# Optimization experiments

Measured on AMD Instinct MI355X. Metric: run time of the kernel, lower is better.

## Reference

```python
import jax, jax.numpy as jnp
from jax import lax
import numpy as np

KERNEL = 3      # patch kernel
RATE = 2        # dilation / downscale rate
SCALE = 10.0    # softmax_scale
EPS = 1e-4


def extract_patches(x, k, s):
    """TF tf.image.extract_patches with SAME padding.
    x: [B,H,W,C] -> [B, oh, ow, k, k, C] with (ky,kx,c) ordering like TF depth."""
    B, H, W, C = x.shape
    oh, ow = -(-H // s), -(-W // s)
    ph = max((oh - 1) * s + k - H, 0)
    pw = max((ow - 1) * s + k - W, 0)
    xp = jnp.pad(x, ((0, 0), (ph // 2, ph - ph // 2), (pw // 2, pw - pw // 2), (0, 0)))
    rows = []
    for ky in range(k):
        cols = [xp[:, ky: ky + (oh - 1) * s + 1: s, kx: kx + (ow - 1) * s + 1: s, :]
                for kx in range(k)]
        rows.append(jnp.stack(cols, axis=3))        # [B,oh,ow,kx,C]
    return jnp.stack(rows, axis=3)                  # [B,oh,ow,ky,kx,C]


def resize_half(x):
    B, H, W, C = x.shape
    return jax.image.resize(x, (B, H // 2, W // 2, C), 'bilinear', antialias=False)


def fuse_diag(a):
    """conv2d of [N,N] image with eye(3) kernel (SAME): out[i,j]=a[i-1,j-1]+a[i,j]+a[i+1,j+1]."""
    p = jnp.pad(a, 1)
    return p[:-2, :-2] + p[1:-1, 1:-1] + p[2:, 2:]


def setup_inputs() -> dict:
    key = jax.random.key(0)
    x = jax.random.normal(key, (4, 96, 96, 128), jnp.float32)
    # binary mask with a central square hole (1 = missing region)
    mask = jnp.zeros((4, 96, 96, 1), jnp.float32).at[:, 24:72, 24:72, :].set(1.0)
    return {"x": x, "mask": mask}


def reference(x, mask):
    B, H, W, C = x.shape
    k, rate = KERNEL, RATE

    # raw patches from full-res x, stride rate -> deconv weights
    raw_p = extract_patches(x, k, rate)                     # [B,h,w,k,k,C]
    h, w = raw_p.shape[1], raw_p.shape[2]
    L = h * w
    raw_w = raw_p.reshape(B, L, k, k, C).transpose(0, 2, 3, 4, 1)   # [B,k,k,C,L]

    # downscaled foreground/background (f == b in this module) and mask
    f = resize_half(x)                                      # [B,h,w,C]
    m = resize_half(mask)                                   # [B,h,w,1]

    wp = extract_patches(f, k, 1).reshape(B, L, k, k, C).transpose(0, 2, 3, 4, 1)  # [B,k,k,C,L]
    mp = extract_patches(m, k, 1).reshape(B, L, -1)         # [B,L,k*k*1]
    mm = (jnp.mean(mp, axis=-1) == 0.0).astype(x.dtype)     # [B,L] valid-patch mask

    fp = extract_patches(f, k, 1)                           # [B,h,w,k,k,C] query patches

    def per_sample(fp_i, wi, raw_wi, mm_i):
        # normalized cross-correlation: conv2d(f_i, wi_normed, SAME)
        norm = jnp.maximum(jnp.sqrt(jnp.sum(wi * wi, axis=(0, 1, 2))), EPS)   # [L]
        wn = wi / norm
        yi = jnp.einsum('hwabc,abcl->hwl', fp_i, wn)        # [h,w,L]

        # diagonal fuse (eye(3) conv) on both patch-grid orderings
        a = fuse_diag(yi.reshape(L, L))
        a = a.reshape(h, w, h, w).transpose(1, 0, 3, 2).reshape(L, L)
        a = fuse_diag(a)
        a = a.reshape(w, h, w, h).transpose(1, 0, 3, 2)     # [h,w,h,w]
        yi = a.reshape(h, w, L)

        # masked softmax over source patches
        yi = yi * mm_i
        yi = jax.nn.softmax(yi * SCALE, axis=-1) * mm_i

        # conv2d_transpose(yi, raw_wi, [1,H,W,C], strides=rate) == vjp of strided conv
        def fwd(z):  # z: [H,W,C] -> [h,w,L]
            return lax.conv_general_dilated(z[None], raw_wi, (rate, rate), 'SAME',
                                            dimension_numbers=('NHWC', 'HWIO', 'NHWC'))[0]
        _, vjp = jax.vjp(fwd, jnp.zeros((H, W, C), x.dtype))
        return vjp(yi)[0] / (rate * rate)                   # [H,W,C]

    return jax.vmap(per_sample)(fp, wp, raw_w, mm)          # [B,H,W,C]
```

## Files before the change

### kernel.cpp

```cpp
#include <hip/hip_runtime.h>
#include <hip/hip_fp16.h>
#include <stdint.h>
#include <string.h>


namespace {

constexpr int B_ = 4;
constexpr int H_ = 96;
constexpr int W_ = 96;
constexpr int C_ = 128;
constexpr int h_ = 48;
constexpr int L_ = 2304;
constexpr int N9_ = 1152;
constexpr int K3_ = 384;
constexpr float SCALE_ = 10.0f;
constexpr float EPS_ = 1e-4f;

constexpr int OUT_F16 = 1;
constexpr int OUT_BF16 = 2;

typedef unsigned short u16;
typedef __attribute__((ext_vector_type(8))) short bfrag8;
typedef __attribute__((ext_vector_type(8))) unsigned short ushort8;
typedef __attribute__((ext_vector_type(4))) unsigned short ushort4v;
typedef __attribute__((ext_vector_type(4))) float f32x4;
typedef __attribute__((ext_vector_type(2))) float f32x2;

__device__ __forceinline__ u16 f2bf(float f) {
  uint32_t x;
  __builtin_memcpy(&x, &f, 4);
  uint32_t lsb = (x >> 16) & 1u;
  x += 0x7fffu + lsb;
  return (u16)(x >> 16);
}
__device__ __forceinline__ float bf2f(u16 u) {
  uint32_t v = ((uint32_t)u) << 16;
  float f;
  __builtin_memcpy(&f, &v, 4);
  return f;
}
__device__ __forceinline__ u16 f2h(float f) {
  __half h = __float2half(f);
  u16 u;
  __builtin_memcpy(&u, &h, 2);
  return u;
}
__device__ __forceinline__ float h2f(u16 u) {
  __half h;
  __builtin_memcpy(&h, &u, 2);
  return __half2float(h);
}

__device__ __forceinline__ void gload16(const u16* g, void* l) {
  __builtin_amdgcn_global_load_lds(
      (const __attribute__((address_space(1))) void*)g,
      (__attribute__((address_space(3))) void*)l, 16, 0, 0);
}

__device__ __forceinline__ int xcd_swz8(int orig, int nwg) {
  int q = nwg >> 3, r = nwg & 7;
  int xcd = orig & 7, pos = orig >> 3;
  return (xcd < r ? xcd * (q + 1) : r * (q + 1) + (xcd - r) * q) + pos;
}

__device__ __forceinline__ uint32_t swzb(uint32_t byte) {
  return byte ^ (((byte >> 7) & 7u) << 4);
}

__global__ __launch_bounds__(128) void k_down(const float* __restrict__ x,
                                              u16* __restrict__ F3a,
                                              u16* __restrict__ F3b,
                                              float* __restrict__ S) {
  int blk = blockIdx.x;
  int b = blk / L_, l = blk % L_;
  int p = l / h_, q = l % h_;
  int c = threadIdx.x;
  const float* xb = x + (((size_t)b * H_ + 2 * p) * W_ + 2 * q) * C_ + c;
  float v = 0.25f * (xb[0] + xb[C_] + xb[(size_t)W_ * C_] + xb[(size_t)W_ * C_ + C_]);
  u16 hi = f2bf(v);
  u16 lo = f2bf(v - bf2f(hi));
  size_t base = ((size_t)b * L_ + l) * K3_;
  F3a[base + c] = hi; F3a[base + 128 + c] = hi; F3a[base + 256 + c] = lo;
  F3b[base + c] = hi; F3b[base + 128 + c] = lo; F3b[base + 256 + c] = hi;
  float ss = v * v;
#pragma unroll
  for (int o = 32; o >= 1; o >>= 1) ss += __shfl_xor(ss, o, 64);
  __shared__ float w2[2];
  if ((c & 63) == 0) w2[c >> 6] = ss;
  __syncthreads();
  if (c == 0) S[(size_t)b * L_ + l] = w2[0] + w2[1];
}

__global__ __launch_bounds__(256) void k_mask(const float* __restrict__ mask,
                                              float* __restrict__ md) {
  int i = blockIdx.x * 256 + threadIdx.x;
  int b = i / L_, l = i % L_, p = l / h_, q = l % h_;
  const float* mb = mask + ((size_t)b * H_ + 2 * p) * W_ + 2 * q;
  md[i] = 0.25f * (mb[0] + mb[1] + mb[W_] + mb[W_ + 1]);
}

__global__ __launch_bounds__(256) void k_mmnorm(const float* __restrict__ S,
                                                const float* __restrict__ md,
                                                float* __restrict__ mm,
                                                float* __restrict__ ninv) {
  int i = blockIdx.x * 256 + threadIdx.x;
  int b = i / L_, l = i % L_, p = l / h_, q = l % h_;
  float ssum = 0.f, msum = 0.f;
#pragma unroll
  for (int a = 0; a < 3; a++) {
    int rp = p - 1 + a;
#pragma unroll
    for (int bb = 0; bb < 3; bb++) {
      int rq = q - 1 + bb;
      bool ok = ((unsigned)rp < (unsigned)h_) && ((unsigned)rq < (unsigned)h_);
      int idx = ok ? (b * L_ + rp * h_ + rq) : 0;
      float sv = S[idx], mv = md[idx];
      if (ok) { ssum += sv; msum += mv; }
    }
  }
  mm[i] = (msum == 0.f) ? 1.f : 0.f;
  float n = fmaxf(sqrtf(ssum), EPS_);
  ninv[i] = 1.f / n;
}

__global__ __launch_bounds__(256) void k_xpack(const float* __restrict__ x,
                                               u16* __restrict__ XpT) {
  int lt = blockIdx.x * 32, jt = blockIdx.y * 64, bz = blockIdx.z;
  __shared__ u16 tile[32][65];
  int t = threadIdx.x;
  int jj = t & 63, lq = t >> 6;
  for (int pass = 0; pass < 8; ++pass) {
    int ll = pass * 4 + lq;
    int l = lt + ll;
    int p = l / h_, q = l % h_;
    int j = jt + jj;
    int a = j / 384, rem = j % 384, bb = rem / 128, c = rem % 128;
    int gy = 2 * p + a, gx = 2 * q + bb;
    float v = 0.f;
    if (gy < H_ && gx < W_) v = x[(((size_t)bz * H_ + gy) * W_ + gx) * C_ + c];
    tile[ll][jj] = f2bf(v);
  }
  __syncthreads();
  int lw = t & 31, jq = t >> 5;
  for (int pass = 0; pass < 8; ++pass) {
    int j2 = pass * 8 + jq;
    XpT[((size_t)bz * N9_ + jt + j2) * L_ + lt + lw] = tile[lw][j2];
  }
}

template <int OUT, bool SYMM>
__global__ __launch_bounds__(256) void gemm_bt(const u16* __restrict__ A,
                                               const u16* __restrict__ B,
                                               void* __restrict__ Cv,
                                               int N, int Kd,
                                               size_t sA, size_t sB, size_t sC) {
  const u16* Ab = A + (size_t)blockIdx.z * sA;
  const u16* Bb = B + (size_t)blockIdx.z * sB;
  int bx, by;
  if (SYMM) {
    int wgid = xcd_swz8(blockIdx.x, gridDim.x);
    int t2 = wgid, row = 0, len = 18;
    while (t2 >= len) { t2 -= len; --len; ++row; }
    by = row;
    bx = row + t2;
  } else {
    int nwg = gridDim.x * gridDim.y;
    int orig = blockIdx.y * gridDim.x + blockIdx.x;
    int wgid = xcd_swz8(orig, nwg);
    bx = wgid % gridDim.x;
    by = wgid / gridDim.x;
  }
  int m0 = by * 128, n0 = bx * 128;

  __shared__ char As[2][8192];
  __shared__ char Bs[2][8192];
  int t = threadIdx.x;
  int lane = t & 63, wv = t >> 6, wr = wv >> 1, wc = wv & 1;
  int mrow = lane & 15, kg = lane >> 4;
  f32x4 acc[4][4];
#pragma unroll
  for (int i = 0; i < 4; i++)
#pragma unroll
    for (int j = 0; j < 4; j++) acc[i][j] = (f32x4)(0.0f);

  uint32_t d16 = (uint32_t)t * 16u;
  uint32_t sz = swzb(d16);
  int rowp = (int)(sz >> 6);
  int kcp = (int)((sz >> 4) & 3u);
  const u16* ga0 = Ab + (size_t)(m0 + rowp) * Kd + kcp * 8;
  const u16* ga1 = Ab + (size_t)(m0 + 64 + rowp) * Kd + kcp * 8;
  const u16* gb0 = Bb + (size_t)(n0 + rowp) * Kd + kcp * 8;
  const u16* gb1 = Bb + (size_t)(n0 + 64 + rowp) * Kd + kcp * 8;

  auto STAGE = [&](int buf, int k0) {
    gload16(ga0 + k0, As[buf] + wv * 1024);
    gload16(ga1 + k0, As[buf] + 4096 + wv * 1024);
    gload16(gb0 + k0, Bs[buf] + wv * 1024);
    gload16(gb1 + k0, Bs[buf] + 4096 + wv * 1024);
  };

  int nsteps = Kd >> 5;
  STAGE(0, 0);
  __syncthreads();
  int cur = 0;
  for (int s = 0; s < nsteps; ++s) {
    if (s + 1 < nsteps) STAGE(cur ^ 1, (s + 1) << 5);
    bfrag8 af[4], bf[4];
#pragma unroll
    for (int i = 0; i < 4; i++) {
      uint32_t byte = (uint32_t)(wr * 64 + i * 16 + mrow) * 64u + (uint32_t)kg * 16u;
      af[i] = *(const bfrag8*)(As[cur] + swzb(byte));
    }
#pragma unroll
    for (int i = 0; i < 4; i++) {
      uint32_t byte = (uint32_t)(wc * 64 + i * 16 + mrow) * 64u + (uint32_t)kg * 16u;
      bf[i] = *(const bfrag8*)(Bs[cur] + swzb(byte));
    }
#pragma unroll
    for (int i = 0; i < 4; i++)
#pragma unroll
      for (int j = 0; j < 4; j++)
        acc[i][j] = __builtin_amdgcn_mfma_f32_16x16x32_bf16(af[i], bf[j], acc[i][j], 0, 0, 0);
    __syncthreads();
    cur ^= 1;
  }
#pragma unroll
  for (int i = 0; i < 4; i++)
#pragma unroll
    for (int j = 0; j < 4; j++)
#pragma unroll
      for (int r = 0; r < 4; r++) {
        int gr = m0 + wr * 64 + i * 16 + kg * 4 + r;
        int gc = n0 + wc * 64 + j * 16 + mrow;
        if (OUT == OUT_BF16) {
          ((u16*)Cv)[(size_t)blockIdx.z * sC + (size_t)gr * N + gc] = f2bf(acc[i][j][r]);
        } else {
          ((u16*)Cv)[(size_t)blockIdx.z * sC + (size_t)gr * N + gc] = f2h(acc[i][j][r]);
        }
      }
  if (SYMM && bx > by) {
    u16* Cb = (u16*)Cv + (size_t)blockIdx.z * sC;
#pragma unroll
    for (int i = 0; i < 4; i++)
#pragma unroll
      for (int j = 0; j < 4; j++) {
        int grb = m0 + wr * 64 + i * 16 + kg * 4;
        int gc = n0 + wc * 64 + j * 16 + mrow;
        ushort4v pk;
#pragma unroll
        for (int r = 0; r < 4; r++) pk[r] = f2h(acc[i][j][r]);
        *(ushort4v*)(Cb + (size_t)gc * N + grb) = pk;
      }
  }
}

template <int S>
__device__ __forceinline__ void tap(const u16* __restrict__ Ub, int o8, bool tok,
                                    const bool* md, int b, float* acc) {
  constexpr int REM = ((S % 8) + 8) % 8;
  int off = tok ? (o8 + S * 2305) : (8 + REM);
  float v[8];
  if constexpr (REM == 0) {
    ushort8 w = *(const ushort8*)(Ub + off);
#pragma unroll
    for (int i = 0; i < 8; i++) v[i] = h2f(w[i]);
  } else if constexpr (REM == 1) {
    ushort8 w = *(const ushort8*)(Ub + off - 1);
    u16 sc = Ub[off + 7];
#pragma unroll
    for (int i = 0; i < 7; i++) v[i] = h2f(w[i + 1]);
    v[7] = h2f(sc);
  } else {
    u16 sc = Ub[off];
    ushort8 w = *(const ushort8*)(Ub + off + 1);
    v[0] = h2f(sc);
#pragma unroll
    for (int i = 1; i < 8; i++) v[i] = h2f(w[i - 1]);
  }
#pragma unroll
  for (int i = 0; i < 8; i++) acc[i] += (tok && md[b + i]) ? v[i] : 0.f;
}

__global__ __launch_bounds__(256) void k_patchsum(const u16* __restrict__ U,
                                                  u16* __restrict__ V,
                                                  const float* __restrict__ ninv,
                                                  int b0) {
  int blk = xcd_swz8(blockIdx.x, gridDim.x);
  int bz = blockIdx.z;
  int o8 = (blk * 256 + (int)threadIdx.x) * 8;
  int R = o8 / L_;
  int col = o8 - R * L_;
  const u16* Ub = U + (size_t)bz * L_ * L_;
  u16* Vb = V + (size_t)bz * L_ * L_;
  int hq = R / h_, wq = R % h_, ps = col / h_, qs0 = col % h_;
  bool ra[3], rb[3], ca[3];
#pragma unroll
  for (int a = 0; a < 3; a++) {
    ra[a] = (unsigned)(hq - 1 + a) < (unsigned)h_;
    rb[a] = (unsigned)(wq - 1 + a) < (unsigned)h_;
    ca[a] = (unsigned)(ps - 1 + a) < (unsigned)h_;
  }
  bool md[10];
#pragma unroll
  for (int d = 0; d < 10; d++) md[d] = (unsigned)(qs0 - 1 + d) < (unsigned)h_;

  float acc[8];
#pragma unroll
  for (int i = 0; i < 8; i++) acc[i] = 0.f;

  bool t0 = ra[0] && ca[0];
  bool t1 = ra[1] && ca[1];
  bool t2 = ra[2] && ca[2];
  tap<-49>(Ub, o8, t0 && rb[0], md, 0, acc);
  tap<-48>(Ub, o8, t0 && rb[1], md, 1, acc);
  tap<-47>(Ub, o8, t0 && rb[2], md, 2, acc);
  tap<-1>(Ub, o8, t1 && rb[0], md, 0, acc);
  tap<0>(Ub, o8, t1 && rb[1], md, 1, acc);
  tap<1>(Ub, o8, t1 && rb[2], md, 2, acc);
  tap<47>(Ub, o8, t2 && rb[0], md, 0, acc);
  tap<48>(Ub, o8, t2 && rb[1], md, 1, acc);
  tap<49>(Ub, o8, t2 && rb[2], md, 2, acc);

  const float* nvb = ninv + (size_t)(b0 + bz) * L_ + col;
  ushort8 ov;
#pragma unroll
  for (int i = 0; i < 8; i++) ov[i] = f2h(acc[i] * nvb[i]);
  *(ushort8*)(Vb + o8) = ov;
}

__global__ __launch_bounds__(256) void k_fsm(const u16* __restrict__ V1,
                                             const float* __restrict__ mm,
                                             u16* __restrict__ Aout,
                                             int b0) {
  int i = xcd_swz8(blockIdx.x, L_), bz = blockIdx.y;
  int hq = i / h_, wq = i % h_;
  const u16* Vb = V1 + (size_t)bz * L_ * L_;
  const float* mmb = mm + (size_t)(b0 + bz) * L_;
  u16* arow = Aout + ((size_t)bz * L_ + i) * L_;
  int t = threadIdx.x;

  uint32_t rowBase[3];
  bool rw0[3], rw1[3], rw2[3];
#pragma unroll
  for (int d2 = 0; d2 < 3; d2++) {
    int TA = wq * h_ + hq + (d2 - 1);
    bool ok = (TA >= 0) && (TA < L_);
    int TAc = ok ? TA : 0;
    int iB = (TAc % h_) * h_ + TAc / h_;
    rowBase[d2] = (uint32_t)(iB * L_);
    rw0[d2] = ok && (iB - 1 >= 0);
    rw1[d2] = ok;
    rw2[d2] = ok && (iB + 1 < L_);
  }
  bool fastR = rw0[0] && rw1[0] && rw2[0] && rw0[1] && rw1[1] && rw2[1] &&
               rw0[2] && rw1[2] && rw2[2];

  float y[9];
  float mx = -3.0e38f;

  auto full_col = [&](int j, int jy) -> float {
    int jB0 = (jy >= 1) ? (j - h_) : (j + (L_ - h_ - 1));
    int jB1 = j;
    int jB2 = (jy <= h_ - 2) ? (j + h_) : (j - (L_ - h_ - 1));
    bool tb0 = (j > 0), tb2 = (j < L_ - 1);
    float s = 0.f;
    {
      uint32_t oc = rowBase[0] + (uint32_t)jB0;
      bool w0 = rw0[0] && tb0 && (jB0 > 0);
      bool w1 = rw1[0] && tb0;
      bool w2 = rw2[0] && tb0 && (jB0 < L_ - 1);
      float vm = h2f(Vb[w0 ? oc - (L_ + 1) : 0u]);
      float vc = h2f(Vb[w1 ? oc : 0u]);
      float vp = h2f(Vb[w2 ? oc + (L_ + 1) : 0u]);
      s += (w0 ? vm : 0.f) + (w1 ? vc : 0.f) + (w2 ? vp : 0.f);
    }
    {
      uint32_t oc = rowBase[1] + (uint32_t)jB1;
      bool w0 = rw0[1] && (jB1 > 0);
      bool w1 = rw1[1];
      bool w2 = rw2[1] && (jB1 < L_ - 1);
      float vm = h2f(Vb[w0 ? oc - (L_ + 1) : 0u]);
      float vc = h2f(Vb[w1 ? oc : 0u]);
      float vp = h2f(Vb[w2 ? oc + (L_ + 1) : 0u]);
      s += (w0 ? vm : 0.f) + (w1 ? vc : 0.f) + (w2 ? vp : 0.f);
    }
    {
      uint32_t oc = rowBase[2] + (uint32_t)jB2;
      bool w0 = rw0[2] && tb2 && (jB2 > 0);
      bool w1 = rw1[2] && tb2;
      bool w2 = rw2[2] && tb2 && (jB2 < L_ - 1);
      float vm = h2f(Vb[w0 ? oc - (L_ + 1) : 0u]);
      float vc = h2f(Vb[w1 ? oc : 0u]);
      float vp = h2f(Vb[w2 ? oc + (L_ + 1) : 0u]);
      s += (w0 ? vm : 0.f) + (w1 ? vc : 0.f) + (w2 ? vp : 0.f);
    }
    return s;
  };

  {
    int j = t;
    float zv = full_col(j, t / h_) * mmb[j] * SCALE_;
    y[0] = zv;
    mx = fmaxf(mx, zv);
  }
  if (fastR) {
#pragma unroll
    for (int cc = 1; cc <= 7; cc++) {
      int j = cc * 256 + t;
      float s = 0.f;
#pragma unroll
      for (int d2 = 0; d2 < 3; d2++) {
        uint32_t oc = rowBase[d2] + (uint32_t)(j + h_ * (d2 - 1));
        s += h2f(Vb[oc - (L_ + 1)]) + h2f(Vb[oc]) + h2f(Vb[oc + (L_ + 1)]);
      }
      float zv = s * mmb[j] * SCALE_;
      y[cc] = zv;
      mx = fmaxf(mx, zv);
    }
  } else {
#pragma unroll
    for (int cc = 1; cc <= 7; cc++) {
      int j = cc * 256 + t;
      float s = 0.f;
#pragma unroll
      for (int d2 = 0; d2 < 3; d2++) {
        uint32_t oc = rowBase[d2] + (uint32_t)(j + h_ * (d2 - 1));
        float vm = h2f(Vb[rw0[d2] ? oc - (L_ + 1) : 0u]);
        float vc = h2f(Vb[rw1[d2] ? oc : 0u]);
        float vp = h2f(Vb[rw2[d2] ? oc + (L_ + 1) : 0u]);
        s += (rw0[d2] ? vm : 0.f) + (rw1[d2] ? vc : 0.f) + (rw2[d2] ? vp : 0.f);
      }
      float zv = s * mmb[j] * SCALE_;
      y[cc] = zv;
      mx = fmaxf(mx, zv);
    }
  }
  {
    int j = 2048 + t;
    float zv = full_col(j, j / h_) * mmb[j] * SCALE_;
    y[8] = zv;
    mx = fmaxf(mx, zv);
  }

  int lane = t & 63, wid = t >> 6;
  __shared__ float wredm[4];
  __shared__ float wreds[4];
#pragma unroll
  for (int o = 32; o >= 1; o >>= 1) mx = fmaxf(mx, __shfl_xor(mx, o, 64));
  if (lane == 0) wredm[wid] = mx;
  __syncthreads();
  float MX = fmaxf(fmaxf(wredm[0], wredm[1]), fmaxf(wredm[2], wredm[3]));
  float sm = 0.f;
#pragma unroll
  for (int cc = 0; cc < 9; cc++) {
    y[cc] = __expf(y[cc] - MX);
    sm += y[cc];
  }
#pragma unroll
  for (int o = 32; o >= 1; o >>= 1) sm += __shfl_xor(sm, o, 64);
  if (lane == 0) wreds[wid] = sm;
  __syncthreads();
  float inv = 1.0f / (wreds[0] + wreds[1] + wreds[2] + wreds[3]);
#pragma unroll
  for (int cc = 0; cc < 9; cc++) {
    int j = cc * 256 + t;
    arow[j] = f2bf(y[cc] * inv * mmb[j]);
  }
}

__global__ __launch_bounds__(256) void k_scatter(const u16* __restrict__ P,
                                                 float* __restrict__ out) {
  int idx = blockIdx.x * 256 + threadIdx.x;
  int c4 = idx & 31;
  int r = idx >> 5;
  int xx = r % W_; r /= W_;
  int y = r % H_;
  int bz = r / H_;
  const u16* Pb = P + (size_t)bz * L_ * N9_;
  int yo[2], ya[2], ny = 0;
  if (y & 1) { yo[0] = y >> 1; ya[0] = 1; ny = 1; }
  else {
    yo[0] = y >> 1; ya[0] = 0; ny = 1;
    if (y >= 2) { yo[1] = (y >> 1) - 1; ya[1] = 2; ny = 2; }
  }
  int xo[2], xa[2], nx = 0;
  if (xx & 1) { xo[0] = xx >> 1; xa[0] = 1; nx = 1; }
  else {
    xo[0] = xx >> 1; xa[0] = 0; nx = 1;
    if (xx >= 2) { xo[1] = (xx >> 1) - 1; xa[1] = 2; nx = 2; }
  }
  float s[4] = {0.f, 0.f, 0.f, 0.f};
  for (int i = 0; i < ny; i++)
    for (int j = 0; j < nx; j++) {
      size_t off = (size_t)(yo[i] * h_ + xo[j]) * N9_ + (ya[i] * 3 + xa[j]) * C_ + 4 * c4;
      ushort4v w = *(const ushort4v*)(Pb + off);
#pragma unroll
      for (int k = 0; k < 4; k++) s[k] += bf2f(w[k]);
    }
  f32x4 o;
#pragma unroll
  for (int k = 0; k < 4; k++) o[k] = 0.25f * s[k];
  *(f32x4*)(out + ((size_t)bz * H_ + y) * (size_t)W_ * C_ + (size_t)xx * C_ + 4 * c4) = o;
}

}

extern "C" void kernel_launch(void* const* d_in, const int* in_sizes, int n_in,
                              void* d_out, int out_size, void* d_ws, size_t ws_size,
                              hipStream_t stream) {
  (void)in_sizes; (void)n_in; (void)out_size;
  const float* x = (const float*)d_in[0];
  const float* mask = (const float*)d_in[1];
  float* out = (float*)d_out;
  char* ws = (char*)d_ws;

  const size_t szF3 = (size_t)B_ * L_ * K3_ * sizeof(u16);
  const size_t szSm = (size_t)B_ * L_ * sizeof(float);
  const size_t off_F3a = 0;
  const size_t off_F3b = off_F3a + szF3;
  const size_t off_S = off_F3b + szF3;
  const size_t off_md = off_S + szSm;
  const size_t off_mm = off_md + szSm;
  const size_t off_nv = off_mm + szSm;
  const size_t off_fixed_end = off_nv + szSm;

  const size_t perXp = (size_t)N9_ * L_ * sizeof(u16);
  const size_t perU = (size_t)L_ * L_ * sizeof(u16);
  const size_t perV = (size_t)L_ * L_ * sizeof(u16);
  int G = 4;
  while (G > 1 && off_fixed_end + (size_t)G * (perXp + perU + perV) > ws_size) G >>= 1;

  const size_t off_XpT = off_fixed_end;
  const size_t off_U = off_XpT + (size_t)G * perXp;
  const size_t off_V = off_U + (size_t)G * perU;

  u16* F3a = (u16*)(ws + off_F3a);
  u16* F3b = (u16*)(ws + off_F3b);
  float* S = (float*)(ws + off_S);
  float* md = (float*)(ws + off_md);
  float* mm = (float*)(ws + off_mm);
  float* nv = (float*)(ws + off_nv);
  u16* XpT = (u16*)(ws + off_XpT);
  u16* U = (u16*)(ws + off_U);
  u16* V = (u16*)(ws + off_V);
  u16* Abuf = (u16*)(ws + off_U);
  u16* Pbuf = (u16*)(ws + off_V);

  k_down<<<dim3(B_ * L_), dim3(C_), 0, stream>>>(x, F3a, F3b, S);
  k_mask<<<dim3((B_ * L_) / 256), dim3(256), 0, stream>>>(mask, md);
  k_mmnorm<<<dim3((B_ * L_) / 256), dim3(256), 0, stream>>>(S, md, mm, nv);

  for (int sb = 0; sb < B_; sb += G) {
    const float* xs = x + (size_t)sb * H_ * W_ * C_;
    k_xpack<<<dim3(L_ / 32, N9_ / 64, G), dim3(256), 0, stream>>>(xs, XpT);
    gemm_bt<OUT_F16, true><<<dim3(171, 1, G), dim3(256), 0, stream>>>(
        F3a + (size_t)sb * L_ * K3_, F3b + (size_t)sb * L_ * K3_, (void*)U,
        L_, K3_, (size_t)L_ * K3_, (size_t)L_ * K3_, (size_t)L_ * L_);
    k_patchsum<<<dim3((L_ * L_) / (256 * 8), 1, G), dim3(256), 0, stream>>>(U, V, nv, sb);
    k_fsm<<<dim3(L_, G), dim3(256), 0, stream>>>(V, mm, Abuf, sb);
    gemm_bt<OUT_BF16, false><<<dim3(N9_ / 128, L_ / 128, G), dim3(256), 0, stream>>>(
        Abuf, XpT, (void*)Pbuf, N9_, L_,
        (size_t)L_ * L_, (size_t)N9_ * L_, (size_t)L_ * N9_);
    k_scatter<<<dim3((G * H_ * W_ * C_ / 4) / 256), dim3(256), 0, stream>>>(
        Pbuf, out + (size_t)sb * H_ * W_ * C_);
  }
}
```

Baseline: 191.3 us.

## Use 144x144-tile 9-wave GEMM for attention-times-patches product

```diff
diff --git a/kernel.cpp b/kernel.cpp
--- a/kernel.cpp
+++ b/kernel.cpp
@@ -173,8 +173,8 @@
   }
   int m0 = by * 128, n0 = bx * 128;
 
-  __shared__ char As[2][8192];
-  __shared__ char Bs[2][8192];
+  __shared__ __align__(128) char As[2][8192];
+  __shared__ __align__(128) char Bs[2][8192];
   int t = threadIdx.x;
   int lane = t & 63, wv = t >> 6, wr = wv >> 1, wc = wv & 1;
   int mrow = lane & 15, kg = lane >> 4;
@@ -253,6 +253,80 @@
         *(ushort4v*)(Cb + (size_t)gc * N + grb) = pk;
       }
   }
+}
+
+__global__ __launch_bounds__(576) void gemm_ap144(const u16* __restrict__ A,
+                                                  const u16* __restrict__ B,
+                                                  u16* __restrict__ Cv,
+                                                  int N, int Kd,
+                                                  size_t sA, size_t sB, size_t sC) {
+  const u16* Ab = A + (size_t)blockIdx.z * sA;
+  const u16* Bb = B + (size_t)blockIdx.z * sB;
+  int nwg = gridDim.x * gridDim.y;
+  int orig = blockIdx.y * gridDim.x + blockIdx.x;
+  int wgid = xcd_swz8(orig, nwg);
+  int bx = wgid % gridDim.x, by = wgid / gridDim.x;
+  int m0 = by * 144, n0 = bx * 144;
+
+  __shared__ __align__(128) char As[2][9216];
+  __shared__ __align__(128) char Bs[2][9216];
+  int t = threadIdx.x;
+  int lane = t & 63, wv = t >> 6;
+  int wrow = wv / 3, wcol = wv % 3;
+  int mrow = lane & 15, kg = lane >> 4;
+  f32x4 acc[3][3];
+#pragma unroll
+  for (int i = 0; i < 3; i++)
+#pragma unroll
+    for (int j = 0; j < 3; j++) acc[i][j] = (f32x4)(0.0f);
+
+  uint32_t d16 = (uint32_t)t * 16u;
+  uint32_t sz = swzb(d16);
+  int rowp = (int)(sz >> 6);
+  int kcp = (int)((sz >> 4) & 3u);
+  const u16* ga = Ab + (size_t)(m0 + rowp) * Kd + kcp * 8;
+  const u16* gb = Bb + (size_t)(n0 + rowp) * Kd + kcp * 8;
+
+  auto STAGE = [&](int buf, int k0) {
+    gload16(ga + k0, As[buf] + wv * 1024);
+    gload16(gb + k0, Bs[buf] + wv * 1024);
+  };
+
+  int nsteps = Kd >> 5;
+  STAGE(0, 0);
+  __syncthreads();
+  int cur = 0;
+  for (int s = 0; s < nsteps; ++s) {
+    if (s + 1 < nsteps) STAGE(cur ^ 1, (s + 1) << 5);
+    bfrag8 af[3], bf[3];
+#pragma unroll
+    for (int i = 0; i < 3; i++) {
+      uint32_t byte = (uint32_t)(wrow * 48 + i * 16 + mrow) * 64u + (uint32_t)kg * 16u;
+      af[i] = *(const bfrag8*)(As[cur] + swzb(byte));
+    }
+#pragma unroll
+    for (int j = 0; j < 3; j++) {
+      uint32_t byte = (uint32_t)(wcol * 48 + j * 16 + mrow) * 64u + (uint32_t)kg * 16u;
+      bf[j] = *(const bfrag8*)(Bs[cur] + swzb(byte));
+    }
+#pragma unroll
+    for (int i = 0; i < 3; i++)
+#pragma unroll
+      for (int j = 0; j < 3; j++)
+        acc[i][j] = __builtin_amdgcn_mfma_f32_16x16x32_bf16(af[i], bf[j], acc[i][j], 0, 0, 0);
+    __syncthreads();
+    cur ^= 1;
+  }
+#pragma unroll
+  for (int i = 0; i < 3; i++)
+#pragma unroll
+    for (int j = 0; j < 3; j++)
+#pragma unroll
+      for (int r = 0; r < 4; r++) {
+        int gr = m0 + wrow * 48 + i * 16 + kg * 4 + r;
+        int gc = n0 + wcol * 48 + j * 16 + mrow;
+        Cv[(size_t)blockIdx.z * sC + (size_t)gr * N + gc] = f2bf(acc[i][j][r]);
+      }
 }
 
 template <int S>
@@ -559,8 +633,8 @@
         L_, K3_, (size_t)L_ * K3_, (size_t)L_ * K3_, (size_t)L_ * L_);
     k_patchsum<<<dim3((L_ * L_) / (256 * 8), 1, G), dim3(256), 0, stream>>>(U, V, nv, sb);
     k_fsm<<<dim3(L_, G), dim3(256), 0, stream>>>(V, mm, Abuf, sb);
-    gemm_bt<OUT_BF16, false><<<dim3(N9_ / 128, L_ / 128, G), dim3(256), 0, stream>>>(
-        Abuf, XpT, (void*)Pbuf, N9_, L_,
+    gemm_ap144<<<dim3(N9_ / 144, L_ / 144, G), dim3(576), 0, stream>>>(
+        Abuf, XpT, Pbuf, N9_, L_,
         (size_t)L_ * L_, (size_t)N9_ * L_, (size_t)L_ * N9_);
     k_scatter<<<dim3((G * H_ * W_ * C_ / 4) / 256), dim3(256), 0, stream>>>(
         Pbuf, out + (size_t)sb * H_ * W_ * C_);
```

Result: faster. 185.9 us (median of 3 runs) (-2.8%).
